# Kernel optimization log

Measured on AMD Instinct MI355X. Metric: run time of the kernel, lower is better.

The kernel has to match this reference:

```python
import jax, jax.numpy as jnp
import numpy as np

DEGREE = 8


def _askey_wilson_basis(x, a, b, c, d, q, degree):
    # Iterative 3-term recurrence (same math as the recursive torch version).
    # x: (batch, input_dim); a,b,c,d,q: scalars broadcast over x.
    basis = [jnp.ones_like(x)]
    if degree >= 1:
        p1 = (2 * (1 + a * b * q) * x - (a + b) * (1 + c * d * q)) / (1 + a * b * c * d * q ** 2)
        basis.append(p1)
    for n in range(2, degree + 1):
        An = (1 - a * b * q ** (n - 1)) * (1 - c * d * q ** (n - 1)) * (1 - a * b * c * d * q ** (2 * n - 2))
        An = An / ((1 - a * b * c * d * q ** (2 * n - 1)) * (1 - a * b * c * d * q ** (2 * n)))
        Cn = (1 - q ** n) * (1 - a * b * q ** (n - 1)) * (1 - c * d * q ** (n - 1)) * (1 - a * b * c * d * q ** (2 * n - 2))
        Cn = Cn / ((1 - a * b * c * d * q ** (2 * n - 2)) * (1 - a * b * c * d * q ** (2 * n - 1)))
        pn = ((2 * x - An) * basis[n - 1] - Cn * basis[n - 2]) / (1 - q ** n)
        basis.append(pn)
    return jnp.stack(basis, axis=-1)  # (batch, input_dim, degree+1)


def setup_inputs() -> dict:
    key = jax.random.key(0)
    k1, k2, k3, k4, k5, k6, k7 = jax.random.split(key, 7)
    input_dim, output_dim, degree = 1024, 1024, DEGREE
    batch = 8192
    x = jax.random.normal(k1, (batch, input_dim), dtype=jnp.float32)
    a = jax.random.normal(k2, (1,), dtype=jnp.float32)
    b = jax.random.normal(k3, (1,), dtype=jnp.float32)
    c = jax.random.normal(k4, (1,), dtype=jnp.float32)
    d = jax.random.normal(k5, (1,), dtype=jnp.float32)
    q = jax.random.normal(k6, (1,), dtype=jnp.float32)
    std = 1.0 / (input_dim * (degree + 1))
    coeffs = jax.random.normal(k7, (input_dim, output_dim, degree + 1), dtype=jnp.float32) * std
    return {"x": x, "a": a, "b": b, "c": c, "d": d, "q": q, "coeffs": coeffs}


def reference(x, a, b, c, d, q, coeffs) -> jnp.ndarray:
    a0, b0, c0, d0, q0 = a[0], b[0], c[0], d[0], q[0]
    basis = _askey_wilson_basis(x, a0, b0, c0, d0, q0, DEGREE)  # (b, i, d+1)
    y = jnp.einsum('bid,iod->bo', basis, coeffs)
    return y
```

## Files before the change

kernel.cpp:

```cpp
#include <hip/hip_runtime.h>
#include <cstdint>

typedef unsigned short u16;
typedef __bf16 bf16x8 __attribute__((ext_vector_type(8)));
typedef float f32x4 __attribute__((ext_vector_type(4)));

#define M_DIM 8192
#define N_DIM 1024
#define I_DIM 1024
#define NDEG 8
#define K_DIM (I_DIM * NDEG)
#define BM 256
#define BN 128
#define BK 64
#define NT (K_DIM / BK)
#define A_TILE (BM * BK)
#define B_TILE (BN * BK)

__device__ __forceinline__ u16 f2bf(float f) {
    union { float f; uint32_t u; } v; v.f = f;
    return (u16)((v.u + 0x7FFFu + ((v.u >> 16) & 1u)) >> 16);
}

__device__ __forceinline__ void gload_lds16(const u16* g, u16* l) {
    auto lp = reinterpret_cast<__attribute__((address_space(3))) uint32_t*>(
        reinterpret_cast<uintptr_t>(l));
    __builtin_amdgcn_global_load_lds(reinterpret_cast<const uint32_t*>(g), lp, 16, 0, 0);
}

__global__ __launch_bounds__(256) void aw_transform(
    const float* __restrict__ coeffs, u16* __restrict__ Bt, float* __restrict__ bias)
{
    __shared__ float lds[32][292];
    int bi = blockIdx.x >> 5, bo = blockIdx.x & 31;
    int i0 = bi * 32, o0 = bo * 32;
    int t = threadIdx.x;

    {
        int r = t >> 3, s = t & 7;
        const float4* src = (const float4*)(coeffs + ((size_t)(i0 + r) * N_DIM + o0) * 9);
#pragma unroll
        for (int j = 0; j < 9; ++j) {
            float4 v = src[s * 9 + j];
            *(float4*)&lds[r][(s * 9 + j) * 4] = v;
        }
    }
    __syncthreads();

    {
        int c = t >> 3, s2 = t & 7;
        u16 ob[32];
#pragma unroll
        for (int rr = 0; rr < 4; ++rr)
#pragma unroll
            for (int dd = 0; dd < 8; ++dd)
                ob[rr * 8 + dd] = f2bf(lds[s2 * 4 + rr][c * 9 + 1 + dd]);
        uint4* dst = (uint4*)(Bt + (size_t)(o0 + c) * K_DIM + (size_t)i0 * 8 + s2 * 32);
        const uint4* sp = (const uint4*)ob;
#pragma unroll
        for (int u = 0; u < 4; ++u) dst[u] = sp[u];
    }

    if (t < 32) {
        float sum = 0.f;
#pragma unroll
        for (int rr = 0; rr < 32; ++rr) sum += lds[rr][t * 9];
        atomicAdd(&bias[o0 + t], sum);
    }
}

__global__ void aw_basis(const float* __restrict__ x,
                         const float* __restrict__ pa, const float* __restrict__ pb,
                         const float* __restrict__ pc, const float* __restrict__ pd,
                         const float* __restrict__ pq,
                         u16* __restrict__ A, int row0)
{
    int t  = blockIdx.x * 256 + threadIdx.x;
    int rb = t >> 7;
    int g  = t & 127;
    int i0 = g << 3;
    int b  = row0 + rb;

    float a = *pa, bb = *pb, c = *pc, d = *pd, q = *pq;
    float ab = a * bb, cd = c * d, abcd = ab * cd;

    float qp[17];
    qp[0] = 1.f;
#pragma unroll
    for (int k = 1; k <= 16; ++k) qp[k] = qp[k - 1] * q;

    float den1 = 1.f + abcd * q * q;
    float c1x = 2.f * (1.f + ab * q) / den1;
    float c1c = -(a + bb) * (1.f + cd * q) / den1;

    float An[9], Cn[9], Sn[9];
#pragma unroll
    for (int n = 2; n <= 8; ++n) {
        float t1 = 1.f - ab * qp[n - 1];
        float t2 = 1.f - cd * qp[n - 1];
        float t3 = 1.f - abcd * qp[2 * n - 2];
        float t4 = 1.f - abcd * qp[2 * n - 1];
        float t5 = 1.f - abcd * qp[2 * n];
        An[n] = (t1 * t2 * t3) / (t4 * t5);
        Cn[n] = ((1.f - qp[n]) * t1 * t2 * t3) / (t3 * t4);
        Sn[n] = 1.f / (1.f - qp[n]);
    }

    const float4* x4 = (const float4*)(x + (size_t)b * I_DIM + i0);
    float4 v0 = x4[0], v1 = x4[1];
    float xv[8] = {v0.x, v0.y, v0.z, v0.w, v1.x, v1.y, v1.z, v1.w};

    u16 ob[64];
#pragma unroll
    for (int j = 0; j < 8; ++j) {
        float xj = xv[j];
        float p1 = c1x * xj + c1c;
        ob[j * 8 + 0] = f2bf(p1);
        float pm2 = 1.f, pm1 = p1;
#pragma unroll
        for (int n = 2; n <= 8; ++n) {
            float pn = ((2.f * xj - An[n]) * pm1 - Cn[n] * pm2) * Sn[n];
            ob[j * 8 + n - 1] = f2bf(pn);
            pm2 = pm1; pm1 = pn;
        }
    }

    uint4* dst = (uint4*)(A + (size_t)rb * K_DIM + (size_t)i0 * 8);
    const uint4* s = (const uint4*)ob;
#pragma unroll
    for (int u = 0; u < 8; ++u) dst[u] = s[u];
}

__global__ __launch_bounds__(512) void aw_gemm(
    const u16* __restrict__ A,
    const u16* __restrict__ B,
    const float* __restrict__ bias,
    float* __restrict__ C,
    int row0, int rowBlocks)
{
    __shared__ alignas(16) u16 As[3 * A_TILE];
    __shared__ alignas(16) u16 Bs[3 * B_TILE];

    int nwg = rowBlocks * 8;
    int bid = blockIdx.x;
    int per = nwg >> 3;
    int logical = (bid & 7) * per + (bid >> 3);
    int rowBlk = logical >> 3;
    int colBlk = logical & 7;

    const int tid  = threadIdx.x;
    const int lane = tid & 63;
    const int wid  = tid >> 6;
    const int wr = wid & 3;
    const int wc = wid >> 2;

    const u16* gA[4]; const u16* gB[2];
    int ldsA[4], ldsB[2];
#pragma unroll
    for (int j = 0; j < 4; ++j) {
        int idx = j * 512 + tid;
        int r = idx >> 3, sl = idx & 7;
        gA[j] = A + (size_t)rowBlk * BM * K_DIM + (size_t)r * K_DIM + ((sl ^ (r & 7)) << 3);
        ldsA[j] = idx << 3;
    }
#pragma unroll
    for (int j = 0; j < 2; ++j) {
        int idx = j * 512 + tid;
        int r = idx >> 3, sl = idx & 7;
        gB[j] = B + (size_t)colBlk * BN * K_DIM + (size_t)r * K_DIM + ((sl ^ (r & 7)) << 3);
        ldsB[j] = idx << 3;
    }

    int offA[2][4], offB[2][4];
#pragma unroll
    for (int ks = 0; ks < 2; ++ks) {
#pragma unroll
        for (int mi = 0; mi < 4; ++mi) {
            int r = wr * 64 + mi * 16 + (lane & 15);
            int s = ks * 4 + (lane >> 4);
            offA[ks][mi] = r * 128 + ((s ^ (r & 7)) << 4);
        }
#pragma unroll
        for (int ni = 0; ni < 4; ++ni) {
            int r = wc * 64 + ni * 16 + (lane & 15);
            int s = ks * 4 + (lane >> 4);
            offB[ks][ni] = r * 128 + ((s ^ (r & 7)) << 4);
        }
    }

    f32x4 acc[4][4];
#pragma unroll
    for (int mi = 0; mi < 4; ++mi)
#pragma unroll
        for (int ni = 0; ni < 4; ++ni)
            acc[mi][ni] = (f32x4){0.f, 0.f, 0.f, 0.f};

    auto stage = [&](int kt, int buf) {
        const int k0 = kt * BK;
        u16* dA = As + buf * A_TILE;
        u16* dB = Bs + buf * B_TILE;
        gload_lds16(gA[0] + k0, dA + ldsA[0]);
        gload_lds16(gA[1] + k0, dA + ldsA[1]);
        gload_lds16(gA[2] + k0, dA + ldsA[2]);
        gload_lds16(gA[3] + k0, dA + ldsA[3]);
        gload_lds16(gB[0] + k0, dB + ldsB[0]);
        gload_lds16(gB[1] + k0, dB + ldsB[1]);
    };

    stage(0, 0);
    stage(1, 1);
    asm volatile("s_waitcnt vmcnt(6)" ::: "memory");
    __builtin_amdgcn_s_barrier();

    int buf = 0;
    for (int t = 0; t < NT; ++t) {
        const char* aB = (const char*)(As + buf * A_TILE);
        const char* bB = (const char*)(Bs + buf * B_TILE);
        int nb = buf + 2; if (nb >= 3) nb -= 3;
        const bool pf = (t + 2 < NT);

        bf16x8 a0[4], b0[4], a1[4], b1[4];
#pragma unroll
        for (int mi = 0; mi < 4; ++mi) a0[mi] = *(const bf16x8*)(aB + offA[0][mi]);
#pragma unroll
        for (int ni = 0; ni < 4; ++ni) b0[ni] = *(const bf16x8*)(bB + offB[0][ni]);
        if (pf) stage(t + 2, nb);
#pragma unroll
        for (int mi = 0; mi < 4; ++mi) a1[mi] = *(const bf16x8*)(aB + offA[1][mi]);
#pragma unroll
        for (int ni = 0; ni < 4; ++ni) b1[ni] = *(const bf16x8*)(bB + offB[1][ni]);

        __builtin_amdgcn_s_setprio(1);
#pragma unroll
        for (int mi = 0; mi < 4; ++mi)
#pragma unroll
            for (int ni = 0; ni < 4; ++ni)
                acc[mi][ni] = __builtin_amdgcn_mfma_f32_16x16x32_bf16(
                    a0[mi], b0[ni], acc[mi][ni], 0, 0, 0);
#pragma unroll
        for (int mi = 0; mi < 4; ++mi)
#pragma unroll
            for (int ni = 0; ni < 4; ++ni)
                acc[mi][ni] = __builtin_amdgcn_mfma_f32_16x16x32_bf16(
                    a1[mi], b1[ni], acc[mi][ni], 0, 0, 0);
        __builtin_amdgcn_s_setprio(0);

        if (pf)              { asm volatile("s_waitcnt vmcnt(6)" ::: "memory"); }
        else if (t + 1 < NT) { asm volatile("s_waitcnt vmcnt(0)" ::: "memory"); }
        __builtin_amdgcn_s_barrier();

        buf += 1; if (buf >= 3) buf -= 3;
    }

    int gRow = row0 + rowBlk * BM + wr * 64;
    int gCol = colBlk * BN + wc * 64;
#pragma unroll
    for (int mi = 0; mi < 4; ++mi) {
#pragma unroll
        for (int ni = 0; ni < 4; ++ni) {
            int rr = gRow + mi * 16 + ((lane >> 4) << 2);
            int cc = gCol + ni * 16 + (lane & 15);
            float bv = bias[cc];
            float* dst = C + (size_t)rr * N_DIM + cc;
#pragma unroll
            for (int j = 0; j < 4; ++j) dst[(size_t)j * N_DIM] = acc[mi][ni][j] + bv;
        }
    }
}

extern "C" void kernel_launch(void* const* d_in, const int* in_sizes, int n_in,
                              void* d_out, int out_size, void* d_ws, size_t ws_size,
                              hipStream_t stream)
{
    const float* x      = (const float*)d_in[0];
    const float* pa     = (const float*)d_in[1];
    const float* pb     = (const float*)d_in[2];
    const float* pc     = (const float*)d_in[3];
    const float* pd     = (const float*)d_in[4];
    const float* pq     = (const float*)d_in[5];
    const float* coeffs = (const float*)d_in[6];
    float* out = (float*)d_out;

    float* bias = (float*)d_ws;
    const size_t biasBytes = 4096;
    u16* Bt = (u16*)((char*)d_ws + biasBytes);
    const size_t btBytes = (size_t)N_DIM * K_DIM * sizeof(u16);
    u16* Abuf = (u16*)((char*)d_ws + biasBytes + btBytes);
    size_t used = biasBytes + btBytes;
    size_t avail = ws_size > used ? ws_size - used : 0;

    int chunk = M_DIM;
    while (chunk > 256 && (size_t)chunk * K_DIM * sizeof(u16) > avail) chunk >>= 1;

    hipMemsetAsync(bias, 0, N_DIM * sizeof(float), stream);
    aw_transform<<<1024, 256, 0, stream>>>(coeffs, Bt, bias);

    for (int row0 = 0; row0 < M_DIM; row0 += chunk) {
        aw_basis<<<(chunk * 128) / 256, 256, 0, stream>>>(x, pa, pb, pc, pd, pq, Abuf, row0);
        int rowBlocks = chunk / BM;
        aw_gemm<<<rowBlocks * 8, 512, 0, stream>>>(Abuf, Bt, bias, out, row0, rowBlocks);
    }
}
```

Baseline: 187.3 us.

## Fuse Askey-Wilson basis generation into GEMM mainloop, dropping A buffer

Removes the separate basis kernel and its bf16 A matrix round-trip through global memory. Each GEMM workgroup now loads raw x, evaluates the recurrence in registers and writes the swizzled bf16 A tile straight into LDS. The B-only pipeline drops from triple to double buffering with __syncthreads. The trade-off is redundant basis computation: each A tile is recomputed by all 8 column blocks. That adds VALU work and serialisation inside the MFMA loop, and the B prefetch distance shrinks.

```diff
diff --git a/kernel.cpp b/kernel.cpp
--- a/kernel.cpp
+++ b/kernel.cpp
@@ -69,31 +69,39 @@
     }
 }
 
-__global__ void aw_basis(const float* __restrict__ x,
-                         const float* __restrict__ pa, const float* __restrict__ pb,
-                         const float* __restrict__ pc, const float* __restrict__ pd,
-                         const float* __restrict__ pq,
-                         u16* __restrict__ A, int row0)
+__global__ __launch_bounds__(512) void aw_gemm(
+    const float* __restrict__ x,
+    const u16* __restrict__ B,
+    const float* __restrict__ pa, const float* __restrict__ pb,
+    const float* __restrict__ pc, const float* __restrict__ pd,
+    const float* __restrict__ pq,
+    const float* __restrict__ bias,
+    float* __restrict__ C)
 {
-    int t  = blockIdx.x * 256 + threadIdx.x;
-    int rb = t >> 7;
-    int g  = t & 127;
-    int i0 = g << 3;
-    int b  = row0 + rb;
+    __shared__ alignas(16) u16 As[2 * A_TILE];
+    __shared__ alignas(16) u16 Bs[2 * B_TILE];
+
+    int bid = blockIdx.x;
+    int logical = (bid & 7) * 32 + (bid >> 3);
+    int rowBlk = logical >> 3;
+    int colBlk = logical & 7;
+
+    const int tid  = threadIdx.x;
+    const int lane = tid & 63;
+    const int wid  = tid >> 6;
+    const int wr = wid & 3;
+    const int wc = wid >> 2;
 
     float a = *pa, bb = *pb, c = *pc, d = *pd, q = *pq;
     float ab = a * bb, cd = c * d, abcd = ab * cd;
-
     float qp[17];
     qp[0] = 1.f;
 #pragma unroll
     for (int k = 1; k <= 16; ++k) qp[k] = qp[k - 1] * q;
-
     float den1 = 1.f + abcd * q * q;
     float c1x = 2.f * (1.f + ab * q) / den1;
     float c1c = -(a + bb) * (1.f + cd * q) / den1;
-
-    float An[9], Cn[9], Sn[9];
+    float An_[9], Cn_[9], Sn_[9];
 #pragma unroll
     for (int n = 2; n <= 8; ++n) {
         float t1 = 1.f - ab * qp[n - 1];
@@ -101,68 +109,13 @@
         float t3 = 1.f - abcd * qp[2 * n - 2];
         float t4 = 1.f - abcd * qp[2 * n - 1];
         float t5 = 1.f - abcd * qp[2 * n];
-        An[n] = (t1 * t2 * t3) / (t4 * t5);
-        Cn[n] = ((1.f - qp[n]) * t1 * t2 * t3) / (t3 * t4);
-        Sn[n] = 1.f / (1.f - qp[n]);
-    }
-
-    const float4* x4 = (const float4*)(x + (size_t)b * I_DIM + i0);
-    float4 v0 = x4[0], v1 = x4[1];
-    float xv[8] = {v0.x, v0.y, v0.z, v0.w, v1.x, v1.y, v1.z, v1.w};
-
-    u16 ob[64];
-#pragma unroll
-    for (int j = 0; j < 8; ++j) {
-        float xj = xv[j];
-        float p1 = c1x * xj + c1c;
-        ob[j * 8 + 0] = f2bf(p1);
-        float pm2 = 1.f, pm1 = p1;
-#pragma unroll
-        for (int n = 2; n <= 8; ++n) {
-            float pn = ((2.f * xj - An[n]) * pm1 - Cn[n] * pm2) * Sn[n];
-            ob[j * 8 + n - 1] = f2bf(pn);
-            pm2 = pm1; pm1 = pn;
-        }
-    }
-
-    uint4* dst = (uint4*)(A + (size_t)rb * K_DIM + (size_t)i0 * 8);
-    const uint4* s = (const uint4*)ob;
-#pragma unroll
-    for (int u = 0; u < 8; ++u) dst[u] = s[u];
-}
-
-__global__ __launch_bounds__(512) void aw_gemm(
-    const u16* __restrict__ A,
-    const u16* __restrict__ B,
-    const float* __restrict__ bias,
-    float* __restrict__ C,
-    int row0, int rowBlocks)
-{
-    __shared__ alignas(16) u16 As[3 * A_TILE];
-    __shared__ alignas(16) u16 Bs[3 * B_TILE];
-
-    int nwg = rowBlocks * 8;
-    int bid = blockIdx.x;
-    int per = nwg >> 3;
-    int logical = (bid & 7) * per + (bid >> 3);
-    int rowBlk = logical >> 3;
-    int colBlk = logical & 7;
-
-    const int tid  = threadIdx.x;
-    const int lane = tid & 63;
-    const int wid  = tid >> 6;
-    const int wr = wid & 3;
-    const int wc = wid >> 2;
-
-    const u16* gA[4]; const u16* gB[2];
-    int ldsA[4], ldsB[2];
-#pragma unroll
-    for (int j = 0; j < 4; ++j) {
-        int idx = j * 512 + tid;
-        int r = idx >> 3, sl = idx & 7;
-        gA[j] = A + (size_t)rowBlk * BM * K_DIM + (size_t)r * K_DIM + ((sl ^ (r & 7)) << 3);
-        ldsA[j] = idx << 3;
-    }
+        An_[n] = (t1 * t2 * t3) / (t4 * t5);
+        Cn_[n] = ((1.f - qp[n]) * t1 * t2 * t3) / (t3 * t4);
+        Sn_[n] = 1.f / (1.f - qp[n]);
+    }
+
+    const u16* gB[2];
+    int ldsB[2];
 #pragma unroll
     for (int j = 0; j < 2; ++j) {
         int idx = j * 512 + tid;
@@ -171,6 +124,11 @@
         ldsB[j] = idx << 3;
     }
 
+    const float4* xp4 = (const float4*)x
+        + (size_t)(rowBlk * BM + (tid >> 1)) * (I_DIM / 4) + (tid & 1);
+    const int arow = tid >> 1;
+    const int sbase = (tid & 1) * 4;
+
     int offA[2][4], offB[2][4];
 #pragma unroll
     for (int ks = 0; ks < 2; ++ks) {
@@ -195,64 +153,99 @@
         for (int ni = 0; ni < 4; ++ni)
             acc[mi][ni] = (f32x4){0.f, 0.f, 0.f, 0.f};
 
-    auto stage = [&](int kt, int buf) {
+    auto stageB = [&](int kt, int buf) {
         const int k0 = kt * BK;
-        u16* dA = As + buf * A_TILE;
         u16* dB = Bs + buf * B_TILE;
-        gload_lds16(gA[0] + k0, dA + ldsA[0]);
-        gload_lds16(gA[1] + k0, dA + ldsA[1]);
-        gload_lds16(gA[2] + k0, dA + ldsA[2]);
-        gload_lds16(gA[3] + k0, dA + ldsA[3]);
         gload_lds16(gB[0] + k0, dB + ldsB[0]);
         gload_lds16(gB[1] + k0, dB + ldsB[1]);
     };
 
-    stage(0, 0);
-    stage(1, 1);
-    asm volatile("s_waitcnt vmcnt(6)" ::: "memory");
-    __builtin_amdgcn_s_barrier();
-
-    int buf = 0;
-    for (int t = 0; t < NT; ++t) {
+    auto computeA = [&](float4 xv, int ab4) {
+        u16* dA = As + ab4 * A_TILE;
+        float xs[4] = {xv.x, xv.y, xv.z, xv.w};
+#pragma unroll
+        for (int j = 0; j < 4; ++j) {
+            float xj = xs[j];
+            bf16x8 v;
+            float p1 = c1x * xj + c1c;
+            v[0] = (__bf16)p1;
+            float pm2 = 1.f, pm1 = p1;
+            float tx = xj + xj;
+#pragma unroll
+            for (int n = 2; n <= 8; ++n) {
+                float pn = ((tx - An_[n]) * pm1 - Cn_[n] * pm2) * Sn_[n];
+                v[n - 1] = (__bf16)pn;
+                pm2 = pm1; pm1 = pn;
+            }
+            int sl = sbase + j;
+            *(bf16x8*)(dA + arow * 64 + ((sl ^ (arow & 7)) << 3)) = v;
+        }
+    };
+
+    auto domfma = [&](int buf) {
         const char* aB = (const char*)(As + buf * A_TILE);
         const char* bB = (const char*)(Bs + buf * B_TILE);
-        int nb = buf + 2; if (nb >= 3) nb -= 3;
-        const bool pf = (t + 2 < NT);
-
         bf16x8 a0[4], b0[4], a1[4], b1[4];
 #pragma unroll
         for (int mi = 0; mi < 4; ++mi) a0[mi] = *(const bf16x8*)(aB + offA[0][mi]);
 #pragma unroll
         for (int ni = 0; ni < 4; ++ni) b0[ni] = *(const bf16x8*)(bB + offB[0][ni]);
-        if (pf) stage(t + 2, nb);
 #pragma unroll
         for (int mi = 0; mi < 4; ++mi) a1[mi] = *(const bf16x8*)(aB + offA[1][mi]);
 #pragma unroll
         for (int ni = 0; ni < 4; ++ni) b1[ni] = *(const bf16x8*)(bB + offB[1][ni]);
-
-        __builtin_amdgcn_s_setprio(1);
-#pragma unroll
-        for (int mi = 0; mi < 4; ++mi)
-#pragma unroll
-            for (int ni = 0; ni < 4; ++ni)
-                acc[mi][ni] = __builtin_amdgcn_mfma_f32_16x16x32_bf16(
-                    a0[mi], b0[ni], acc[mi][ni], 0, 0, 0);
-#pragma unroll
-        for (int mi = 0; mi < 4; ++mi)
-#pragma unroll
-            for (int ni = 0; ni < 4; ++ni)
-                acc[mi][ni] = __builtin_amdgcn_mfma_f32_16x16x32_bf16(
-                    a1[mi], b1[ni], acc[mi][ni], 0, 0, 0);
-        __builtin_amdgcn_s_setprio(0);
-
-        if (pf)              { asm volatile("s_waitcnt vmcnt(6)" ::: "memory"); }
-        else if (t + 1 < NT) { asm volatile("s_waitcnt vmcnt(0)" ::: "memory"); }
-        __builtin_amdgcn_s_barrier();
-
-        buf += 1; if (buf >= 3) buf -= 3;
-    }
-
-    int gRow = row0 + rowBlk * BM + wr * 64;
+        return (void)0, (void)a0, (void)0;
+    };
+    (void)domfma;
+
+    stageB(0, 0);
+    float4 xP = xp4[0];
+    computeA(xP, 0);
+    float4 xN = xp4[2 + 0 * 0];
+    __syncthreads();
+
+#define ITER(T, XC, XN_)                                                      \
+    do {                                                                      \
+        const bool doA = (T) + 1 < NT;                                        \
+        const bool doX = (T) + 2 < NT;                                        \
+        if (doA) stageB((T) + 1, ((T) + 1) & 1);                              \
+        if (doX) XN_ = xp4[((T) + 2) * 2];                                    \
+        const char* aB = (const char*)(As + ((T) & 1) * A_TILE);              \
+        const char* bB = (const char*)(Bs + ((T) & 1) * B_TILE);              \
+        bf16x8 a0[4], b0[4], a1[4], b1[4];                                    \
+        _Pragma("unroll")                                                     \
+        for (int mi = 0; mi < 4; ++mi) a0[mi] = *(const bf16x8*)(aB + offA[0][mi]); \
+        _Pragma("unroll")                                                     \
+        for (int ni = 0; ni < 4; ++ni) b0[ni] = *(const bf16x8*)(bB + offB[0][ni]); \
+        _Pragma("unroll")                                                     \
+        for (int mi = 0; mi < 4; ++mi) a1[mi] = *(const bf16x8*)(aB + offA[1][mi]); \
+        _Pragma("unroll")                                                     \
+        for (int ni = 0; ni < 4; ++ni) b1[ni] = *(const bf16x8*)(bB + offB[1][ni]); \
+        if (doA) computeA(XC, ((T) + 1) & 1);                                 \
+        __builtin_amdgcn_s_setprio(1);                                        \
+        _Pragma("unroll")                                                     \
+        for (int mi = 0; mi < 4; ++mi)                                        \
+            _Pragma("unroll")                                                 \
+            for (int ni = 0; ni < 4; ++ni)                                    \
+                acc[mi][ni] = __builtin_amdgcn_mfma_f32_16x16x32_bf16(        \
+                    a0[mi], b0[ni], acc[mi][ni], 0, 0, 0);                    \
+        _Pragma("unroll")                                                     \
+        for (int mi = 0; mi < 4; ++mi)                                        \
+            _Pragma("unroll")                                                 \
+            for (int ni = 0; ni < 4; ++ni)                                    \
+                acc[mi][ni] = __builtin_amdgcn_mfma_f32_16x16x32_bf16(        \
+                    a1[mi], b1[ni], acc[mi][ni], 0, 0, 0);                    \
+        __builtin_amdgcn_s_setprio(0);                                        \
+        if ((T) + 1 < NT) __syncthreads();                                    \
+    } while (0)
+
+    for (int t = 0; t < NT; t += 2) {
+        ITER(t, xN, xP);
+        ITER(t + 1, xP, xN);
+    }
+#undef ITER
+
+    int gRow = rowBlk * BM + wr * 64;
     int gCol = colBlk * BN + wc * 64;
 #pragma unroll
     for (int mi = 0; mi < 4; ++mi) {
@@ -284,20 +277,8 @@
     float* bias = (float*)d_ws;
     const size_t biasBytes = 4096;
     u16* Bt = (u16*)((char*)d_ws + biasBytes);
-    const size_t btBytes = (size_t)N_DIM * K_DIM * sizeof(u16);
-    u16* Abuf = (u16*)((char*)d_ws + biasBytes + btBytes);
-    size_t used = biasBytes + btBytes;
-    size_t avail = ws_size > used ? ws_size - used : 0;
-
-    int chunk = M_DIM;
-    while (chunk > 256 && (size_t)chunk * K_DIM * sizeof(u16) > avail) chunk >>= 1;
 
     hipMemsetAsync(bias, 0, N_DIM * sizeof(float), stream);
     aw_transform<<<1024, 256, 0, stream>>>(coeffs, Bt, bias);
-
-    for (int row0 = 0; row0 < M_DIM; row0 += chunk) {
-        aw_basis<<<(chunk * 128) / 256, 256, 0, stream>>>(x, pa, pb, pc, pd, pq, Abuf, row0);
-        int rowBlocks = chunk / BM;
-        aw_gemm<<<rowBlocks * 8, 512, 0, stream>>>(Abuf, Bt, bias, out, row0, rowBlocks);
-    }
-}
+    aw_gemm<<<256, 512, 0, stream>>>(x, Bt, pa, pb, pc, pd, pq, bias, out);
+}
```

Result: slower. 215.2 us (+14.9%).

## Shrink GEMM tile to 128x128 with double buffering and fuse prep kernels

Applied to the files above, without the earlier changes.

Halves the GEMM block tile to 128x128 with 256 threads and a two-stage LDS buffer in place of three stages, and issues the next tile's load at the top of each iteration. The coefficient transform and basis expansion are merged into one prep launch when the workspace can hold the full A matrix. The aim is higher occupancy, more workgroups to fill the CUs, and one fewer launch, at the cost of lower arithmetic intensity per tile and a shallower prefetch pipeline.

```diff
diff --git a/kernel.cpp b/kernel.cpp
--- a/kernel.cpp
+++ b/kernel.cpp
@@ -10,7 +10,7 @@
 #define I_DIM 1024
 #define NDEG 8
 #define K_DIM (I_DIM * NDEG)
-#define BM 256
+#define BM 128
 #define BN 128
 #define BK 64
 #define NT (K_DIM / BK)
@@ -28,13 +28,12 @@
     __builtin_amdgcn_global_load_lds(reinterpret_cast<const uint32_t*>(g), lp, 16, 0, 0);
 }
 
-__global__ __launch_bounds__(256) void aw_transform(
-    const float* __restrict__ coeffs, u16* __restrict__ Bt, float* __restrict__ bias)
-{
-    __shared__ float lds[32][292];
-    int bi = blockIdx.x >> 5, bo = blockIdx.x & 31;
+__device__ __forceinline__ void do_transform_block(
+    int blk, int t, const float* __restrict__ coeffs,
+    u16* __restrict__ Bt, float* __restrict__ bias, float (*lds)[292])
+{
+    int bi = blk >> 5, bo = blk & 31;
     int i0 = bi * 32, o0 = bo * 32;
-    int t = threadIdx.x;
 
     {
         int r = t >> 3, s = t & 7;
@@ -69,15 +68,14 @@
     }
 }
 
-__global__ void aw_basis(const float* __restrict__ x,
-                         const float* __restrict__ pa, const float* __restrict__ pb,
-                         const float* __restrict__ pc, const float* __restrict__ pd,
-                         const float* __restrict__ pq,
-                         u16* __restrict__ A, int row0)
-{
-    int t  = blockIdx.x * 256 + threadIdx.x;
-    int rb = t >> 7;
-    int g  = t & 127;
+__device__ __forceinline__ void do_basis_thread(
+    int gt, const float* __restrict__ x,
+    const float* __restrict__ pa, const float* __restrict__ pb,
+    const float* __restrict__ pc, const float* __restrict__ pd,
+    const float* __restrict__ pq, u16* __restrict__ A, int row0)
+{
+    int rb = gt >> 7;
+    int g  = gt & 127;
     int i0 = g << 3;
     int b  = row0 + rb;
 
@@ -131,15 +129,49 @@
     for (int u = 0; u < 8; ++u) dst[u] = s[u];
 }
 
-__global__ __launch_bounds__(512) void aw_gemm(
+__global__ __launch_bounds__(256) void aw_prep(
+    const float* __restrict__ coeffs, const float* __restrict__ x,
+    const float* __restrict__ pa, const float* __restrict__ pb,
+    const float* __restrict__ pc, const float* __restrict__ pd,
+    const float* __restrict__ pq,
+    u16* __restrict__ Bt, float* __restrict__ bias, u16* __restrict__ A)
+{
+    __shared__ float lds[32][292];
+    int blk = blockIdx.x;
+    int t = threadIdx.x;
+    if (blk < 1024) {
+        do_transform_block(blk, t, coeffs, Bt, bias, lds);
+    } else {
+        int gt = (blk - 1024) * 256 + t;
+        do_basis_thread(gt, x, pa, pb, pc, pd, pq, A, 0);
+    }
+}
+
+__global__ __launch_bounds__(256) void aw_transform(
+    const float* __restrict__ coeffs, u16* __restrict__ Bt, float* __restrict__ bias)
+{
+    __shared__ float lds[32][292];
+    do_transform_block(blockIdx.x, threadIdx.x, coeffs, Bt, bias, lds);
+}
+
+__global__ void aw_basis(const float* __restrict__ x,
+                         const float* __restrict__ pa, const float* __restrict__ pb,
+                         const float* __restrict__ pc, const float* __restrict__ pd,
+                         const float* __restrict__ pq,
+                         u16* __restrict__ A, int row0)
+{
+    do_basis_thread(blockIdx.x * 256 + threadIdx.x, x, pa, pb, pc, pd, pq, A, row0);
+}
+
+__global__ __launch_bounds__(256) void aw_gemm(
     const u16* __restrict__ A,
     const u16* __restrict__ B,
     const float* __restrict__ bias,
     float* __restrict__ C,
     int row0, int rowBlocks)
 {
-    __shared__ alignas(16) u16 As[3 * A_TILE];
-    __shared__ alignas(16) u16 Bs[3 * B_TILE];
+    __shared__ alignas(16) u16 As[2 * A_TILE];
+    __shared__ alignas(16) u16 Bs[2 * B_TILE];
 
     int nwg = rowBlocks * 8;
     int bid = blockIdx.x;
@@ -151,22 +183,17 @@
     const int tid  = threadIdx.x;
     const int lane = tid & 63;
     const int wid  = tid >> 6;
-    const int wr = wid & 3;
-    const int wc = wid >> 2;
-
-    const u16* gA[4]; const u16* gB[2];
-    int ldsA[4], ldsB[2];
+    const int wr = wid >> 1;
+    const int wc = wid & 1;
+
+    const u16* gA[4]; const u16* gB[4];
+    int ldsA[4], ldsB[4];
 #pragma unroll
     for (int j = 0; j < 4; ++j) {
-        int idx = j * 512 + tid;
+        int idx = j * 256 + tid;
         int r = idx >> 3, sl = idx & 7;
         gA[j] = A + (size_t)rowBlk * BM * K_DIM + (size_t)r * K_DIM + ((sl ^ (r & 7)) << 3);
         ldsA[j] = idx << 3;
-    }
-#pragma unroll
-    for (int j = 0; j < 2; ++j) {
-        int idx = j * 512 + tid;
-        int r = idx >> 3, sl = idx & 7;
         gB[j] = B + (size_t)colBlk * BN * K_DIM + (size_t)r * K_DIM + ((sl ^ (r & 7)) << 3);
         ldsB[j] = idx << 3;
     }
@@ -205,26 +232,26 @@
         gload_lds16(gA[3] + k0, dA + ldsA[3]);
         gload_lds16(gB[0] + k0, dB + ldsB[0]);
         gload_lds16(gB[1] + k0, dB + ldsB[1]);
+        gload_lds16(gB[2] + k0, dB + ldsB[2]);
+        gload_lds16(gB[3] + k0, dB + ldsB[3]);
     };
 
     stage(0, 0);
-    stage(1, 1);
-    asm volatile("s_waitcnt vmcnt(6)" ::: "memory");
+    asm volatile("s_waitcnt vmcnt(0)" ::: "memory");
     __builtin_amdgcn_s_barrier();
 
-    int buf = 0;
     for (int t = 0; t < NT; ++t) {
-        const char* aB = (const char*)(As + buf * A_TILE);
-        const char* bB = (const char*)(Bs + buf * B_TILE);
-        int nb = buf + 2; if (nb >= 3) nb -= 3;
-        const bool pf = (t + 2 < NT);
+        const bool pf = (t + 1 < NT);
+        if (pf) stage(t + 1, (t + 1) & 1);
+
+        const char* aB = (const char*)(As + (t & 1) * A_TILE);
+        const char* bB = (const char*)(Bs + (t & 1) * B_TILE);
 
         bf16x8 a0[4], b0[4], a1[4], b1[4];
 #pragma unroll
         for (int mi = 0; mi < 4; ++mi) a0[mi] = *(const bf16x8*)(aB + offA[0][mi]);
 #pragma unroll
         for (int ni = 0; ni < 4; ++ni) b0[ni] = *(const bf16x8*)(bB + offB[0][ni]);
-        if (pf) stage(t + 2, nb);
 #pragma unroll
         for (int mi = 0; mi < 4; ++mi) a1[mi] = *(const bf16x8*)(aB + offA[1][mi]);
 #pragma unroll
@@ -245,11 +272,10 @@
                     a1[mi], b1[ni], acc[mi][ni], 0, 0, 0);
         __builtin_amdgcn_s_setprio(0);
 
-        if (pf)              { asm volatile("s_waitcnt vmcnt(6)" ::: "memory"); }
-        else if (t + 1 < NT) { asm volatile("s_waitcnt vmcnt(0)" ::: "memory"); }
-        __builtin_amdgcn_s_barrier();
-
-        buf += 1; if (buf >= 3) buf -= 3;
+        if (pf) {
+            asm volatile("s_waitcnt vmcnt(0)" ::: "memory");
+            __builtin_amdgcn_s_barrier();
+        }
     }
 
     int gRow = row0 + rowBlk * BM + wr * 64;
@@ -288,16 +314,21 @@
     u16* Abuf = (u16*)((char*)d_ws + biasBytes + btBytes);
     size_t used = biasBytes + btBytes;
     size_t avail = ws_size > used ? ws_size - used : 0;
-
-    int chunk = M_DIM;
-    while (chunk > 256 && (size_t)chunk * K_DIM * sizeof(u16) > avail) chunk >>= 1;
+    const size_t aFullBytes = (size_t)M_DIM * K_DIM * sizeof(u16);
 
     hipMemsetAsync(bias, 0, N_DIM * sizeof(float), stream);
-    aw_transform<<<1024, 256, 0, stream>>>(coeffs, Bt, bias);
-
-    for (int row0 = 0; row0 < M_DIM; row0 += chunk) {
-        aw_basis<<<(chunk * 128) / 256, 256, 0, stream>>>(x, pa, pb, pc, pd, pq, Abuf, row0);
-        int rowBlocks = chunk / BM;
-        aw_gemm<<<rowBlocks * 8, 512, 0, stream>>>(Abuf, Bt, bias, out, row0, rowBlocks);
-    }
-}
+
+    if (avail >= aFullBytes) {
+        aw_prep<<<1024 + (M_DIM * 128) / 256, 256, 0, stream>>>(
+            coeffs, x, pa, pb, pc, pd, pq, Bt, bias, Abuf);
+        aw_gemm<<<(M_DIM / BM) * 8, 256, 0, stream>>>(Abuf, Bt, bias, out, 0, M_DIM / BM);
+    } else {
+        int chunk = M_DIM;
+        while (chunk > 256 && (size_t)chunk * K_DIM * sizeof(u16) > avail) chunk >>= 1;
+        aw_transform<<<1024, 256, 0, stream>>>(coeffs, Bt, bias);
+        for (int row0 = 0; row0 < M_DIM; row0 += chunk) {
+            aw_basis<<<(chunk * 128) / 256, 256, 0, stream>>>(x, pa, pb, pc, pd, pq, Abuf, row0);
+            aw_gemm<<<(chunk / BM) * 8, 256, 0, stream>>>(Abuf, Bt, bias, out, row0, chunk / BM);
+        }
+    }
+}
```

Result: slower. 201.4 us (+7.6%).
